# Performance work log

Measured on AMD Instinct MI355X. Metric: run time of the kernel, lower is better.

## Reference

```python
import jax, jax.numpy as jnp
import numpy as np

N, E, F, HID, HEADS, G = 20000, 320000, 64, 64, 4, 64
HC = HEADS * HID  # 256
NHID, NOUT = 256, 128
INV_SQRT2 = 0.7071067811865476


def _gat(x, src, dst, W, a_s, a_d, bias):
    # GATConv (v1), eval mode (no dropout); src/dst already include self-loops (PyG default)
    H, C = a_s.shape
    h = (x @ W).reshape(-1, H, C)  # [N,H,C]
    al_s = jnp.einsum('nhc,hc->nh', h, a_s)
    al_d = jnp.einsum('nhc,hc->nh', h, a_d)
    e = jax.nn.leaky_relu(al_s[src] + al_d[dst], 0.2)  # [Etot,H]
    m = jax.ops.segment_max(e, dst, num_segments=N)
    ex = jnp.exp(e - m[dst])
    den = jax.ops.segment_sum(ex, dst, num_segments=N)
    coef = ex / den[dst]  # softmax over incoming edges per target node
    out = jax.ops.segment_sum(h[src] * coef[:, :, None], dst, num_segments=N)
    return out.reshape(-1, H * C) + bias


def _bn(h, g, b):
    # BatchNorm1d, training-mode stats (biased var), eps=1e-5
    mu = h.mean(axis=0)
    var = h.var(axis=0)
    return g * (h - mu) * jax.lax.rsqrt(var + 1e-5) + b


def _block(x, src, dst, W1, a1s, a1d, b1, g1, be1, W2, a2s, a2d, b2, g2, be2, Wr, br, Wf, bf):
    h = jax.nn.relu(_bn(_gat(x, src, dst, W1, a1s, a1d, b1), g1, be1))
    h = jax.nn.relu(_bn(_gat(h, src, dst, W2, a2s, a2d, b2), g2, be2))
    res = x @ Wr + br
    return ((h + res) * INV_SQRT2) @ Wf + bf


def setup_inputs():
    ks = iter(jax.random.split(jax.random.key(0), 64))
    def rn(shape, scale=0.05):
        return jax.random.normal(next(ks), shape, dtype=jnp.float32) * scale
    inp = {}
    inp['x'] = jax.random.normal(next(ks), (N, F), dtype=jnp.float32)
    inp['edge_index'] = jax.random.randint(next(ks), (2, E), 0, N, dtype=jnp.int32)
    inp['batch'] = jnp.sort(jax.random.randint(next(ks), (N,), 0, G, dtype=jnp.int32))
    for b, cin in enumerate([F, HID]):
        p = 'b%d_' % b
        inp[p + 'W1'] = rn((cin, HC)); inp[p + 'a1s'] = rn((HEADS, HID)); inp[p + 'a1d'] = rn((HEADS, HID))
        inp[p + 'b1'] = jnp.zeros((HC,), jnp.float32)
        inp[p + 'g1'] = jnp.ones((HC,), jnp.float32); inp[p + 'be1'] = jnp.zeros((HC,), jnp.float32)
        inp[p + 'W2'] = rn((HC, HC)); inp[p + 'a2s'] = rn((1, HC)); inp[p + 'a2d'] = rn((1, HC))
        inp[p + 'b2'] = jnp.zeros((HC,), jnp.float32)
        inp[p + 'g2'] = jnp.ones((HC,), jnp.float32); inp[p + 'be2'] = jnp.zeros((HC,), jnp.float32)
        inp[p + 'Wr'] = rn((cin, HC)); inp[p + 'br'] = jnp.zeros((HC,), jnp.float32)
        inp[p + 'Wf'] = rn((HC, HID)); inp[p + 'bf'] = jnp.zeros((HID,), jnp.float32)
    inp['Wh1'] = rn((HID, NHID)); inp['bh1'] = jnp.zeros((NHID,), jnp.float32)
    inp['Wh2'] = rn((NHID, NOUT)); inp['bh2'] = jnp.zeros((NOUT,), jnp.float32)
    return inp


def reference(x, edge_index, batch,
              b0_W1, b0_a1s, b0_a1d, b0_b1, b0_g1, b0_be1, b0_W2, b0_a2s, b0_a2d, b0_b2, b0_g2, b0_be2, b0_Wr, b0_br, b0_Wf, b0_bf,
              b1_W1, b1_a1s, b1_a1d, b1_b1, b1_g1, b1_be1, b1_W2, b1_a2s, b1_a2d, b1_b2, b1_g2, b1_be2, b1_Wr, b1_br, b1_Wf, b1_bf,
              Wh1, bh1, Wh2, bh2):
    loops = jnp.arange(N, dtype=edge_index.dtype)
    src = jnp.concatenate([edge_index[0], loops])
    dst = jnp.concatenate([edge_index[1], loops])
    x = _block(x, src, dst, b0_W1, b0_a1s, b0_a1d, b0_b1, b0_g1, b0_be1, b0_W2, b0_a2s, b0_a2d, b0_b2, b0_g2, b0_be2, b0_Wr, b0_br, b0_Wf, b0_bf)
    x = _block(x, src, dst, b1_W1, b1_a1s, b1_a1d, b1_b1, b1_g1, b1_be1, b1_W2, b1_a2s, b1_a2d, b1_b2, b1_g2, b1_be2, b1_Wr, b1_br, b1_Wf, b1_bf)
    cnt = jax.ops.segment_sum(jnp.ones((N,), x.dtype), batch, num_segments=G)
    pooled = jax.ops.segment_sum(x, batch, num_segments=G) / jnp.maximum(cnt, 1.0)[:, None]
    h = jax.nn.relu(pooled @ Wh1 + bh1)
    return h @ Wh2 + bh2
```

## Files before the change

### kernel.cpp

```cpp
#include <hip/hip_runtime.h>

#define N_NODES 20000
#define N_EDGES 320000
#define ETOT (N_EDGES + N_NODES)
#define G_GROUPS 64
#define BN_BLOCKS 256
#define BN_BANKS 8

typedef __attribute__((ext_vector_type(8))) short bf16x8;
typedef __attribute__((ext_vector_type(4))) float f32x4;

__device__ __forceinline__ unsigned short f2bf(float f) {
    unsigned int u = __float_as_uint(f);
    u += 0x7fffu + ((u >> 16) & 1u);
    return (unsigned short)(u >> 16);
}
__device__ __forceinline__ float bf2f(unsigned short v) {
    return __uint_as_float(((unsigned int)v) << 16);
}
__device__ __forceinline__ unsigned int pack2bf(float a, float b) {
    return (unsigned int)f2bf(a) | ((unsigned int)f2bf(b) << 16);
}


__global__ __launch_bounds__(256) void k_hist(const int* __restrict__ ei, int* __restrict__ counts) {
    int e = blockIdx.x * 256 + threadIdx.x;
    if (e >= ETOT) return;
    int dst = (e < N_EDGES) ? ei[N_EDGES + e] : (e - N_EDGES);
    atomicAdd(&counts[dst], 1);
}

__global__ __launch_bounds__(1024) void k_scan(const int* __restrict__ counts, int* __restrict__ offs,
                                               int* __restrict__ cursor) {
    __shared__ int sdata[1024];
    const int t = threadIdx.x;
    const int chunk = (N_NODES + 1023) / 1024;
    int base = t * chunk;
    int s = 0;
    for (int i = 0; i < chunk; i++) { int idx = base + i; if (idx < N_NODES) s += counts[idx]; }
    sdata[t] = s;
    __syncthreads();
    for (int off = 1; off < 1024; off <<= 1) {
        int v = (t >= off) ? sdata[t - off] : 0;
        __syncthreads();
        sdata[t] += v;
        __syncthreads();
    }
    int prefix = (t == 0) ? 0 : sdata[t - 1];
    for (int i = 0; i < chunk; i++) {
        int idx = base + i;
        if (idx < N_NODES) {
            int cv = counts[idx];
            offs[idx] = prefix;
            cursor[idx] = prefix;
            prefix += cv;
        }
    }
    if (t == 1023) offs[N_NODES] = sdata[1023];
}

__global__ __launch_bounds__(256) void k_scatter(const int* __restrict__ ei, int* __restrict__ cursor,
                                                 int* __restrict__ csr_src) {
    int e = blockIdx.x * 256 + threadIdx.x;
    if (e >= ETOT) return;
    int src = (e < N_EDGES) ? ei[e] : (e - N_EDGES);
    int dst = (e < N_EDGES) ? ei[N_EDGES + e] : (e - N_EDGES);
    int p = atomicAdd(&cursor[dst], 1);
    csr_src[p] = src;
}


__global__ __launch_bounds__(256) void k_prepB_all(const float* __restrict__ W2a, const float* __restrict__ W2b,
                                                   const float* __restrict__ W1a, const float* __restrict__ Wra,
                                                   const float* __restrict__ W1b, const float* __restrict__ Wrb,
                                                   unsigned short* __restrict__ B2a, unsigned short* __restrict__ B2b,
                                                   unsigned short* __restrict__ B1a, unsigned short* __restrict__ Bra,
                                                   unsigned short* __restrict__ B1b, unsigned short* __restrict__ Brb) {
    int b = blockIdx.x;
    const float* W;
    unsigned short* Bf;
    int s0;
    if (b < 32) { W = W2a; Bf = B2a; s0 = b; }
    else if (b < 64) { W = W2b; Bf = B2b; s0 = b - 32; }
    else if (b < 72) { W = W1a; Bf = B1a; s0 = b - 64; }
    else if (b < 80) { W = Wra; Bf = Bra; s0 = b - 72; }
    else if (b < 88) { W = W1b; Bf = B1b; s0 = b - 80; }
    else { W = Wrb; Bf = Brb; s0 = b - 88; }
    int s = s0 * 256 + threadIdx.x;
    int l = s & 63;
    int nt = (s >> 6) & 15;
    int kt = s >> 10;
    int n = nt * 16 + (l & 15);
    int kb = kt * 32 + (l >> 4) * 8;
    float v[8];
    #pragma unroll
    for (int j = 0; j < 8; j++) v[j] = W[(kb + j) * 256 + n];
    uint4 q = {pack2bf(v[0], v[1]), pack2bf(v[2], v[3]), pack2bf(v[4], v[5]), pack2bf(v[6], v[7])};
    *(uint4*)(Bf + s * 8) = q;
}


__global__ __launch_bounds__(256) void k_gemm64_dual(const float* __restrict__ x,
                                                     const unsigned short* __restrict__ Bf1,
                                                     const unsigned short* __restrict__ Bfr,
                                                     const float* __restrict__ br,
                                                     const float* __restrict__ a_s, const float* __restrict__ a_d,
                                                     unsigned short* __restrict__ hbf, float* __restrict__ res,
                                                     float* __restrict__ alS, float* __restrict__ alD) {
    const int rb = blockIdx.x >> 2, cs = blockIdx.x & 3;
    const int row0 = rb * 64;
    const int nrows = min(64, N_NODES - row0);
    const int t = threadIdx.x;
    const int w = t >> 6;
    const int l = t & 63;
    const int quad = l >> 4;
    const int colLocal = l & 15;
    __shared__ unsigned short As[8 * 64 * 8];
    __shared__ float alsm[4][64], aldm[4][64];

    const int ntg = cs * 4 + w;
    bf16x8 b1f[2], brf[2];
    #pragma unroll
    for (int kt = 0; kt < 2; kt++) {
        b1f[kt] = *(const bf16x8*)(Bf1 + ((kt * 16 + ntg) * 64 + l) * 8);
        brf[kt] = *(const bf16x8*)(Bfr + ((kt * 16 + ntg) * 64 + l) * 8);
    }

    #pragma unroll
    for (int gi = 0; gi < 2; gi++) {
        int g = 2 * w + gi;
        int kt = g >> 2, mt = g & 3;
        int sm = mt * 16 + (l & 15);
        int koff = kt * 32 + (l >> 4) * 8;
        float4 v0 = {0.f, 0.f, 0.f, 0.f}, v1 = {0.f, 0.f, 0.f, 0.f};
        if (sm < nrows) {
            v0 = *(const float4*)(x + (row0 + sm) * 64 + koff);
            v1 = *(const float4*)(x + (row0 + sm) * 64 + koff + 4);
        }
        uint4 q = {pack2bf(v0.x, v0.y), pack2bf(v0.z, v0.w), pack2bf(v1.x, v1.y), pack2bf(v1.z, v1.w)};
        *(uint4*)(As + (g * 64 + l) * 8) = q;
    }
    __syncthreads();

    f32x4 acc1[4], acc2[4];
    #pragma unroll
    for (int mt = 0; mt < 4; mt++) {
        acc1[mt] = (f32x4){0.f, 0.f, 0.f, 0.f};
        acc2[mt] = (f32x4){0.f, 0.f, 0.f, 0.f};
    }
    #pragma unroll
    for (int kt = 0; kt < 2; kt++) {
        #pragma unroll
        for (int mt = 0; mt < 4; mt++) {
            bf16x8 af = *(const bf16x8*)(As + ((kt * 4 + mt) * 64 + l) * 8);
            acc1[mt] = __builtin_amdgcn_mfma_f32_16x16x32_bf16(af, b1f[kt], acc1[mt], 0, 0, 0);
            acc2[mt] = __builtin_amdgcn_mfma_f32_16x16x32_bf16(af, brf[kt], acc2[mt], 0, 0, 0);
        }
    }

    const int col = cs * 64 + w * 16 + colLocal;
    const float brv = br[col];
    const float asv = a_s[col];
    const float adv = a_d[col];
    #pragma unroll
    for (int mt = 0; mt < 4; mt++) {
        #pragma unroll
        for (int r = 0; r < 4; r++) {
            float v1 = acc1[mt][r];
            int lr = mt * 16 + quad * 4 + r;
            bool ok = lr < nrows;
            int row = row0 + lr;
            if (ok) {
                hbf[row * 256 + col] = f2bf(v1);
                res[row * 256 + col] = acc2[mt][r] + brv;
            }
            float ps = v1 * asv, pd = v1 * adv;
            #pragma unroll
            for (int off = 1; off < 16; off <<= 1) {
                ps += __shfl_xor(ps, off);
                pd += __shfl_xor(pd, off);
            }
            if (colLocal == 0) {
                alsm[w][lr] = ps;
                aldm[w][lr] = pd;
            }
        }
    }
    __syncthreads();
    if (t < 64 && t < nrows) {
        float s = (alsm[0][t] + alsm[1][t]) + (alsm[2][t] + alsm[3][t]);
        float d = (aldm[0][t] + aldm[1][t]) + (aldm[2][t] + aldm[3][t]);
        alS[(row0 + t) * 4 + cs] = s;
        alD[(row0 + t) * 4 + cs] = d;
    }
}


template <int H>
__global__ __launch_bounds__(256) void k_agg(const unsigned short* __restrict__ hbf, const float* __restrict__ alS,
                                             const float* __restrict__ alD, const int* __restrict__ offs,
                                             const int* __restrict__ csr_src, const float* __restrict__ bias,
                                             float* __restrict__ out) {
    const int node = __builtin_amdgcn_readfirstlane(blockIdx.x * 4 + (threadIdx.x >> 6));
    const int lane = threadIdx.x & 63;
    const int head = (H == 4) ? (lane >> 4) : 0;
    float ald;
    if (H == 4) {
        float4 d4 = *(const float4*)(alD + node * 4);
        ald = (head == 0) ? d4.x : (head == 1) ? d4.y : (head == 2) ? d4.z : d4.w;
    } else {
        ald = alD[node];
    }
    const int e0 = offs[node], e1 = offs[node + 1];
    const unsigned short* hp = hbf + lane * 4;
    float den = 0.f, a0 = 0.f, a1 = 0.f, a2 = 0.f, a3 = 0.f;
    int e = e0;
    for (; e + 16 <= e1; e += 16) {
        int s[16];
        #pragma unroll
        for (int i = 0; i < 16; i++) s[i] = csr_src[e + i];
        ushort4 hq[16];
        #pragma unroll
        for (int i = 0; i < 16; i++) hq[i] = *(const ushort4*)(hp + s[i] * 256);
        float w[16];
        #pragma unroll
        for (int i = 0; i < 16; i++) {
            float v;
            if (H == 4) {
                float4 s4 = *(const float4*)(alS + s[i] * 4);
                float as = (head == 0) ? s4.x : (head == 1) ? s4.y : (head == 2) ? s4.z : s4.w;
                v = as + ald;
            } else {
                v = alS[s[i]] + ald;
            }
            v = (v > 0.f) ? v : 0.2f * v;
            w[i] = __expf(v);
        }
        #pragma unroll
        for (int i = 0; i < 16; i++) {
            den += w[i];
            a0 += w[i] * bf2f(hq[i].x); a1 += w[i] * bf2f(hq[i].y);
            a2 += w[i] * bf2f(hq[i].z); a3 += w[i] * bf2f(hq[i].w);
        }
    }
    for (; e < e1; e++) {
        int s = csr_src[e];
        float v;
        if (H == 4) {
            float4 s4 = *(const float4*)(alS + s * 4);
            float as = (head == 0) ? s4.x : (head == 1) ? s4.y : (head == 2) ? s4.z : s4.w;
            v = as + ald;
        } else {
            v = alS[s] + ald;
        }
        v = (v > 0.f) ? v : 0.2f * v;
        float w = __expf(v);
        ushort4 hq = *(const ushort4*)(hp + s * 256);
        den += w;
        a0 += w * bf2f(hq.x); a1 += w * bf2f(hq.y); a2 += w * bf2f(hq.z); a3 += w * bf2f(hq.w);
    }
    float inv = 1.f / den;
    const float4 bv = *(const float4*)(bias + lane * 4);
    float4 o = {a0 * inv + bv.x, a1 * inv + bv.y, a2 * inv + bv.z, a3 * inv + bv.w};
    *(float4*)(out + node * 256 + lane * 4) = o;
}


__global__ __launch_bounds__(256) void k_bnstats_fin(const float* __restrict__ x, float* __restrict__ sumR,
                                                     float* __restrict__ sumsqR, const float* __restrict__ g,
                                                     const float* __restrict__ be, float* __restrict__ scale,
                                                     float* __restrict__ shift, int* __restrict__ counter,
                                                     float* __restrict__ zS, float* __restrict__ zD) {
    const int c = threadIdx.x;
    const int bank = blockIdx.x & (BN_BANKS - 1);
    if (zS) {
        int idx = blockIdx.x * 256 + c;
        if (idx < N_NODES) { zS[idx] = 0.f; zD[idx] = 0.f; }
    }
    float s = 0.f, q = 0.f;
    int r = blockIdx.x;
    for (; r + 3 * BN_BLOCKS < N_NODES; r += 4 * BN_BLOCKS) {
        float v0 = x[r * 256 + c];
        float v1 = x[(r + BN_BLOCKS) * 256 + c];
        float v2 = x[(r + 2 * BN_BLOCKS) * 256 + c];
        float v3 = x[(r + 3 * BN_BLOCKS) * 256 + c];
        s += (v0 + v1) + (v2 + v3);
        q += (v0 * v0 + v1 * v1) + (v2 * v2 + v3 * v3);
    }
    for (; r < N_NODES; r += BN_BLOCKS) {
        float v = x[r * 256 + c];
        s += v; q += v * v;
    }
    atomicAdd(&sumR[bank * 256 + c], s);
    atomicAdd(&sumsqR[bank * 256 + c], q);
    __threadfence();
    __syncthreads();
    __shared__ int lastFlag;
    if (c == 0) lastFlag = (atomicAdd(counter, 1) == (int)gridDim.x - 1);
    __syncthreads();
    if (lastFlag) {
        float S = 0.f, Q = 0.f;
        #pragma unroll
        for (int k = 0; k < BN_BANKS; k++) {
            S += atomicAdd(&sumR[k * 256 + c], 0.f);
            Q += atomicAdd(&sumsqR[k * 256 + c], 0.f);
        }
        float mu = S * (1.f / N_NODES);
        float var = Q * (1.f / N_NODES) - mu * mu;
        float sc = g[c] * rsqrtf(var + 1e-5f);
        scale[c] = sc;
        shift[c] = be[c] - mu * sc;
        #pragma unroll
        for (int k = 0; k < BN_BANKS; k++) {
            sumR[k * 256 + c] = 0.f;
            sumsqR[k * 256 + c] = 0.f;
        }
        if (c == 0) *counter = 0;
    }
}


__global__ __launch_bounds__(256) void k_gemm256_mfma(const float* __restrict__ A, const float* __restrict__ scale,
                                                      const float* __restrict__ shift,
                                                      const unsigned short* __restrict__ Bf,
                                                      const float* __restrict__ a_s, const float* __restrict__ a_d,
                                                      unsigned short* __restrict__ C, float* __restrict__ alS2,
                                                      float* __restrict__ alD2) {
    const int rb = blockIdx.x >> 2, cs = blockIdx.x & 3;
    const int row0 = rb * 64;
    const int nrows = min(64, N_NODES - row0);
    const int t = threadIdx.x;
    const int w = t >> 6;
    const int l = t & 63;
    const int quad = l >> 4;
    const int colLocal = l & 15;
    __shared__ unsigned short As[2 * 4 * 64 * 8];
    __shared__ float scs[256], shs[256];
    scs[t] = scale[t];
    shs[t] = shift[t];

    const int ntg = cs * 4 + w;
    bf16x8 bfrag[8];
    #pragma unroll
    for (int kt = 0; kt < 8; kt++)
        bfrag[kt] = *(const bf16x8*)(Bf + ((kt * 16 + ntg) * 64 + l) * 8);

    f32x4 acc[4];
    #pragma unroll
    for (int mt = 0; mt < 4; mt++) acc[mt] = (f32x4){0.f, 0.f, 0.f, 0.f};

    const int smt = (t >> 6) & 3;
    const int sm = smt * 16 + (l & 15);
    const int skoff = (l >> 4) * 8;

    for (int kc = 0; kc < 4; kc++) {
        __syncthreads();
        #pragma unroll
        for (int kt2 = 0; kt2 < 2; kt2++) {
            int k = kc * 64 + kt2 * 32 + skoff;
            float4 v0 = {0.f, 0.f, 0.f, 0.f}, v1 = {0.f, 0.f, 0.f, 0.f};
            if (sm < nrows) {
                v0 = *(const float4*)(A + (row0 + sm) * 256 + k);
                v1 = *(const float4*)(A + (row0 + sm) * 256 + k + 4);
                v0.x = fmaxf(v0.x * scs[k + 0] + shs[k + 0], 0.f);
                v0.y = fmaxf(v0.y * scs[k + 1] + shs[k + 1], 0.f);
                v0.z = fmaxf(v0.z * scs[k + 2] + shs[k + 2], 0.f);
                v0.w = fmaxf(v0.w * scs[k + 3] + shs[k + 3], 0.f);
                v1.x = fmaxf(v1.x * scs[k + 4] + shs[k + 4], 0.f);
                v1.y = fmaxf(v1.y * scs[k + 5] + shs[k + 5], 0.f);
                v1.z = fmaxf(v1.z * scs[k + 6] + shs[k + 6], 0.f);
                v1.w = fmaxf(v1.w * scs[k + 7] + shs[k + 7], 0.f);
            }
            uint4 q = {pack2bf(v0.x, v0.y), pack2bf(v0.z, v0.w), pack2bf(v1.x, v1.y), pack2bf(v1.z, v1.w)};
            *(uint4*)(As + ((kt2 * 4 + smt) * 64 + l) * 8) = q;
        }
        __syncthreads();
        #pragma unroll
        for (int kt2 = 0; kt2 < 2; kt2++) {
            int ktg = kc * 2 + kt2;
            #pragma unroll
            for (int mt = 0; mt < 4; mt++) {
                bf16x8 af = *(const bf16x8*)(As + ((kt2 * 4 + mt) * 64 + l) * 8);
                acc[mt] = __builtin_amdgcn_mfma_f32_16x16x32_bf16(af, bfrag[ktg], acc[mt], 0, 0, 0);
            }
        }
    }

    const int col = cs * 64 + w * 16 + colLocal;
    const float asv = a_s[col];
    const float adv = a_d[col];
    #pragma unroll
    for (int mt = 0; mt < 4; mt++) {
        #pragma unroll
        for (int r = 0; r < 4; r++) {
            float v = acc[mt][r];
            int lr = mt * 16 + quad * 4 + r;
            bool ok = lr < nrows;
            int row = row0 + lr;
            if (ok) C[row * 256 + col] = f2bf(v);
            float ps = v * asv, pd = v * adv;
            #pragma unroll
            for (int off = 1; off < 16; off <<= 1) {
                ps += __shfl_xor(ps, off);
                pd += __shfl_xor(pd, off);
            }
            if (colLocal == 0 && ok) {
                atomicAdd(&alS2[row], ps);
                atomicAdd(&alD2[row], pd);
            }
        }
    }
}


__global__ __launch_bounds__(256) void k_gemm_final(const float* __restrict__ A, const float* __restrict__ scale,
                                                    const float* __restrict__ shift, const float* __restrict__ res,
                                                    const float* __restrict__ B, const float* __restrict__ bias,
                                                    float* __restrict__ y) {
    const int row0 = blockIdx.x * 32;
    const int t = threadIdx.x;
    const float INVS = 0.70710678118654752440f;
    __shared__ float xs[32 * 36];
    __shared__ float bs[32 * 64];
    __shared__ float scs[256], shs[256];
    scs[t] = scale[t];
    shs[t] = shift[t];
    const int rf = (t & 15) | ((t >> 7) << 4);
    const int cf = (t >> 4) & 7;
    const int c0 = (t & 15) * 4;
    const int r0 = (t >> 4) * 2;
    float acc[2][4] = {};
    for (int k0 = 0; k0 < 256; k0 += 32) {
        __syncthreads();
        {
            int kcol = k0 + cf * 4;
            int gi = (row0 + rf) * 256 + kcol;
            float4 v = *(const float4*)(A + gi);
            float4 rv = *(const float4*)(res + gi);
            xs[(cf * 4 + 0) * 36 + rf] = (fmaxf(v.x * scs[kcol + 0] + shs[kcol + 0], 0.f) + rv.x) * INVS;
            xs[(cf * 4 + 1) * 36 + rf] = (fmaxf(v.y * scs[kcol + 1] + shs[kcol + 1], 0.f) + rv.y) * INVS;
            xs[(cf * 4 + 2) * 36 + rf] = (fmaxf(v.z * scs[kcol + 2] + shs[kcol + 2], 0.f) + rv.z) * INVS;
            xs[(cf * 4 + 3) * 36 + rf] = (fmaxf(v.w * scs[kcol + 3] + shs[kcol + 3], 0.f) + rv.w) * INVS;
        }
        {
            int cc = (t & 15) * 4;
            int k = t >> 4;
            #pragma unroll
            for (int pass = 0; pass < 2; pass++, k += 16) {
                *(float4*)(bs + k * 64 + cc) = *(const float4*)(B + (k0 + k) * 64 + cc);
            }
        }
        __syncthreads();
        #pragma unroll 8
        for (int k = 0; k < 32; k++) {
            float2 av = *(const float2*)(xs + k * 36 + r0);
            float4 bv = *(const float4*)(bs + k * 64 + c0);
            acc[0][0] += av.x * bv.x; acc[0][1] += av.x * bv.y;
            acc[0][2] += av.x * bv.z; acc[0][3] += av.x * bv.w;
            acc[1][0] += av.y * bv.x; acc[1][1] += av.y * bv.y;
            acc[1][2] += av.y * bv.z; acc[1][3] += av.y * bv.w;
        }
    }
    float4 bv = *(const float4*)(bias + c0);
    #pragma unroll
    for (int i = 0; i < 2; i++) {
        int gr = row0 + r0 + i;
        float4 o = {acc[i][0] + bv.x, acc[i][1] + bv.y, acc[i][2] + bv.z, acc[i][3] + bv.w};
        *(float4*)(y + gr * 64 + c0) = o;
    }
}


__global__ __launch_bounds__(256) void k_pool_head(const float* __restrict__ x, const int* __restrict__ batch,
                                                   const float* __restrict__ Wh1, const float* __restrict__ bh1,
                                                   const float* __restrict__ Wh2, const float* __restrict__ bh2,
                                                   float* __restrict__ out) {
    const int g = blockIdx.x;
    const int t = threadIdx.x;
    int lo = 0, hi = N_NODES;
    while (lo < hi) { int mid = (lo + hi) >> 1; if (batch[mid] < g) lo = mid + 1; else hi = mid; }
    int start = lo;
    hi = N_NODES;
    while (lo < hi) { int mid = (lo + hi) >> 1; if (batch[mid] < g + 1) lo = mid + 1; else hi = mid; }
    int end = lo;
    float cnt = (float)(end - start);

    __shared__ float part[256];
    __shared__ float p[64];
    __shared__ float hrow[256];
    const int c = t & 63;
    float s = 0.f;
    for (int r = start + (t >> 6); r < end; r += 4) s += x[r * 64 + c];
    part[t] = s;
    __syncthreads();
    if (t < 64) {
        float v = part[t] + part[t + 64] + part[t + 128] + part[t + 192];
        p[t] = v / fmaxf(cnt, 1.f);
    }
    __syncthreads();
    float a = bh1[t];
    #pragma unroll 8
    for (int k = 0; k < 64; k++) a += p[k] * Wh1[k * 256 + t];
    hrow[t] = fmaxf(a, 0.f);
    __syncthreads();
    if (t < 128) {
        float o = bh2[t];
        #pragma unroll 8
        for (int k = 0; k < 256; k++) o += hrow[k] * Wh2[k * 128 + t];
        out[g * 128 + t] = o;
    }
}


extern "C" void kernel_launch(void* const* d_in, const int* in_sizes, int n_in,
                              void* d_out, int out_size, void* d_ws, size_t ws_size,
                              hipStream_t stream) {
    (void)in_sizes; (void)n_in; (void)out_size; (void)ws_size;
    const float* x0 = (const float*)d_in[0];
    const int* ei = (const int*)d_in[1];
    const int* batch = (const int*)d_in[2];
    const float* Wh1 = (const float*)d_in[35];
    const float* bh1 = (const float*)d_in[36];
    const float* Wh2 = (const float*)d_in[37];
    const float* bh2 = (const float*)d_in[38];

    char* p = (char*)d_ws;
    auto alloc = [&](size_t bytes) -> void* {
        void* r = (void*)p;
        p += (bytes + 255) & ~(size_t)255;
        return r;
    };
    int* counts = (int*)alloc((size_t)N_NODES * 4);
    float* sumR = (float*)alloc(BN_BANKS * 256 * 4);
    float* sumsqR = (float*)alloc(BN_BANKS * 256 * 4);
    int* bncnt = (int*)alloc(256);
    const size_t zero_bytes = (((size_t)N_NODES * 4 + 255) & ~(size_t)255) + BN_BANKS * 256 * 4 * 2 + 256;
    int* offs = (int*)alloc((size_t)(N_NODES + 1) * 4);
    int* cursor = (int*)alloc((size_t)N_NODES * 4);
    int* csr_src = (int*)alloc((size_t)ETOT * 4);
    float* alS = (float*)alloc((size_t)N_NODES * 4 * 4);
    float* alD = (float*)alloc((size_t)N_NODES * 4 * 4);
    float* alS2 = (float*)alloc((size_t)N_NODES * 4);
    float* alD2 = (float*)alloc((size_t)N_NODES * 4);
    float* scaleb = (float*)alloc(1024);
    float* shiftb = (float*)alloc(1024);
    unsigned short* hbuf = (unsigned short*)alloc((size_t)N_NODES * 256 * 2);
    float* obuf = (float*)alloc((size_t)N_NODES * 256 * 4);
    float* rbuf = (float*)alloc((size_t)N_NODES * 256 * 4);
    float* xout = (float*)alloc((size_t)N_NODES * 64 * 4);
    unsigned short* Bf2_0 = (unsigned short*)alloc(256 * 256 * 2);
    unsigned short* Bf2_1 = (unsigned short*)alloc(256 * 256 * 2);
    unsigned short* Bf1_0 = (unsigned short*)alloc(64 * 256 * 2);
    unsigned short* Bfr_0 = (unsigned short*)alloc(64 * 256 * 2);
    unsigned short* Bf1_1 = (unsigned short*)alloc(64 * 256 * 2);
    unsigned short* Bfr_1 = (unsigned short*)alloc(64 * 256 * 2);

    hipMemsetAsync(counts, 0, zero_bytes, stream);
    k_hist<<<(ETOT + 255) / 256, 256, 0, stream>>>(ei, counts);
    k_scan<<<1, 1024, 0, stream>>>(counts, offs, cursor);
    k_scatter<<<(ETOT + 255) / 256, 256, 0, stream>>>(ei, cursor, csr_src);
    k_prepB_all<<<96, 256, 0, stream>>>((const float*)d_in[3 + 6], (const float*)d_in[19 + 6],
                                        (const float*)d_in[3 + 0], (const float*)d_in[3 + 12],
                                        (const float*)d_in[19 + 0], (const float*)d_in[19 + 12],
                                        Bf2_0, Bf2_1, Bf1_0, Bfr_0, Bf1_1, Bfr_1);

    const int tile64_blocks = ((N_NODES + 63) / 64) * 4;
    const int node_blocks = N_NODES / 4;
    const int final_blocks = N_NODES / 32;

    auto run_block = [&](const float* xin, int base, const unsigned short* Bf2,
                         const unsigned short* Bf1, const unsigned short* Bfr) {
        const float* a1s = (const float*)d_in[base + 1];
        const float* a1d = (const float*)d_in[base + 2];
        const float* b1 = (const float*)d_in[base + 3];
        const float* g1 = (const float*)d_in[base + 4];
        const float* be1 = (const float*)d_in[base + 5];
        const float* a2s = (const float*)d_in[base + 7];
        const float* a2d = (const float*)d_in[base + 8];
        const float* b2 = (const float*)d_in[base + 9];
        const float* g2 = (const float*)d_in[base + 10];
        const float* be2 = (const float*)d_in[base + 11];
        const float* br = (const float*)d_in[base + 13];
        const float* Wf = (const float*)d_in[base + 14];
        const float* bf = (const float*)d_in[base + 15];

        k_gemm64_dual<<<tile64_blocks, 256, 0, stream>>>(xin, Bf1, Bfr, br, a1s, a1d, hbuf, rbuf, alS, alD);
        k_agg<4><<<node_blocks, 256, 0, stream>>>(hbuf, alS, alD, offs, csr_src, b1, obuf);
        k_bnstats_fin<<<BN_BLOCKS, 256, 0, stream>>>(obuf, sumR, sumsqR, g1, be1, scaleb, shiftb, bncnt, alS2, alD2);
        k_gemm256_mfma<<<tile64_blocks, 256, 0, stream>>>(obuf, scaleb, shiftb, Bf2, a2s, a2d, hbuf, alS2, alD2);
        k_agg<1><<<node_blocks, 256, 0, stream>>>(hbuf, alS2, alD2, offs, csr_src, b2, obuf);
        k_bnstats_fin<<<BN_BLOCKS, 256, 0, stream>>>(obuf, sumR, sumsqR, g2, be2, scaleb, shiftb, bncnt, nullptr, nullptr);
        k_gemm_final<<<final_blocks, 256, 0, stream>>>(obuf, scaleb, shiftb, rbuf, Wf, bf, xout);
    };

    run_block(x0, 3, Bf2_0, Bf1_0, Bfr_0);
    run_block(xout, 19, Bf2_1, Bf1_1, Bfr_1);

    k_pool_head<<<G_GROUPS, 256, 0, stream>>>(xout, batch, Wh1, bh1, Wh2, bh2, (float*)d_out);
}
```

Measured before the change: 591.0 us.

## Fuse BatchNorm statistics into GAT aggregation kernel with two-level completion counter

Removes the separate BN-stats kernel. Each aggregation block now reduces its four nodes' outputs and squares in shared memory and atomically adds them into banked partial sums. A per-bank counter followed by a master counter picks the last block, which finalizes scale and shift. This avoids re-reading the 20000x256 fp32 aggregation output and saves one launch per layer. In exchange, all 5000 blocks now issue 512 float atomics each, which may cause contention on the 8 banks.

```diff
diff --git a/kernel.cpp b/kernel.cpp
--- a/kernel.cpp
+++ b/kernel.cpp
@@ -4,7 +4,6 @@
 #define N_EDGES 320000
 #define ETOT (N_EDGES + N_NODES)
 #define G_GROUPS 64
-#define BN_BLOCKS 256
 #define BN_BANKS 8
 
 typedef __attribute__((ext_vector_type(8))) short bf16x8;
@@ -197,13 +196,24 @@
 
 
 template <int H>
-__global__ __launch_bounds__(256) void k_agg(const unsigned short* __restrict__ hbf, const float* __restrict__ alS,
-                                             const float* __restrict__ alD, const int* __restrict__ offs,
-                                             const int* __restrict__ csr_src, const float* __restrict__ bias,
-                                             float* __restrict__ out) {
+__global__ __launch_bounds__(256) void k_agg_bn(const unsigned short* __restrict__ hbf,
+                                               const float* __restrict__ alS, const float* __restrict__ alD,
+                                               const int* __restrict__ offs, const int* __restrict__ csr_src,
+                                               const float* __restrict__ bias, float* __restrict__ out,
+                                               float* __restrict__ sumR, float* __restrict__ sumsqR,
+                                               const float* __restrict__ g, const float* __restrict__ be,
+                                               float* __restrict__ scale, float* __restrict__ shift,
+                                               int* __restrict__ cntBank, int* __restrict__ cntMaster,
+                                               float* __restrict__ zS, float* __restrict__ zD) {
     const int node = __builtin_amdgcn_readfirstlane(blockIdx.x * 4 + (threadIdx.x >> 6));
-    const int lane = threadIdx.x & 63;
+    const int t = threadIdx.x;
+    const int lane = t & 63;
+    const int w = t >> 6;
     const int head = (H == 4) ? (lane >> 4) : 0;
+    __shared__ float lsum[4][256], lqsum[4][256];
+
+    if (H == 4 && lane == 0) { zS[node] = 0.f; zD[node] = 0.f; }
+
     float ald;
     if (H == 4) {
         float4 d4 = *(const float4*)(alD + node * 4);
@@ -222,7 +232,7 @@
         ushort4 hq[16];
         #pragma unroll
         for (int i = 0; i < 16; i++) hq[i] = *(const ushort4*)(hp + s[i] * 256);
-        float w[16];
+        float wq[16];
         #pragma unroll
         for (int i = 0; i < 16; i++) {
             float v;
@@ -234,13 +244,13 @@
                 v = alS[s[i]] + ald;
             }
             v = (v > 0.f) ? v : 0.2f * v;
-            w[i] = __expf(v);
+            wq[i] = __expf(v);
         }
         #pragma unroll
         for (int i = 0; i < 16; i++) {
-            den += w[i];
-            a0 += w[i] * bf2f(hq[i].x); a1 += w[i] * bf2f(hq[i].y);
-            a2 += w[i] * bf2f(hq[i].z); a3 += w[i] * bf2f(hq[i].w);
+            den += wq[i];
+            a0 += wq[i] * bf2f(hq[i].x); a1 += wq[i] * bf2f(hq[i].y);
+            a2 += wq[i] * bf2f(hq[i].z); a3 += wq[i] * bf2f(hq[i].w);
         }
     }
     for (; e < e1; e++) {
@@ -254,51 +264,40 @@
             v = alS[s] + ald;
         }
         v = (v > 0.f) ? v : 0.2f * v;
-        float w = __expf(v);
+        float wv = __expf(v);
         ushort4 hq = *(const ushort4*)(hp + s * 256);
-        den += w;
-        a0 += w * bf2f(hq.x); a1 += w * bf2f(hq.y); a2 += w * bf2f(hq.z); a3 += w * bf2f(hq.w);
+        den += wv;
+        a0 += wv * bf2f(hq.x); a1 += wv * bf2f(hq.y); a2 += wv * bf2f(hq.z); a3 += wv * bf2f(hq.w);
     }
     float inv = 1.f / den;
     const float4 bv = *(const float4*)(bias + lane * 4);
     float4 o = {a0 * inv + bv.x, a1 * inv + bv.y, a2 * inv + bv.z, a3 * inv + bv.w};
     *(float4*)(out + node * 256 + lane * 4) = o;
-}
-
-
-__global__ __launch_bounds__(256) void k_bnstats_fin(const float* __restrict__ x, float* __restrict__ sumR,
-                                                     float* __restrict__ sumsqR, const float* __restrict__ g,
-                                                     const float* __restrict__ be, float* __restrict__ scale,
-                                                     float* __restrict__ shift, int* __restrict__ counter,
-                                                     float* __restrict__ zS, float* __restrict__ zD) {
-    const int c = threadIdx.x;
+
+    *(float4*)(&lsum[w][lane * 4]) = o;
+    float4 q2 = {o.x * o.x, o.y * o.y, o.z * o.z, o.w * o.w};
+    *(float4*)(&lqsum[w][lane * 4]) = q2;
+    __syncthreads();
     const int bank = blockIdx.x & (BN_BANKS - 1);
-    if (zS) {
-        int idx = blockIdx.x * 256 + c;
-        if (idx < N_NODES) { zS[idx] = 0.f; zD[idx] = 0.f; }
-    }
-    float s = 0.f, q = 0.f;
-    int r = blockIdx.x;
-    for (; r + 3 * BN_BLOCKS < N_NODES; r += 4 * BN_BLOCKS) {
-        float v0 = x[r * 256 + c];
-        float v1 = x[(r + BN_BLOCKS) * 256 + c];
-        float v2 = x[(r + 2 * BN_BLOCKS) * 256 + c];
-        float v3 = x[(r + 3 * BN_BLOCKS) * 256 + c];
-        s += (v0 + v1) + (v2 + v3);
-        q += (v0 * v0 + v1 * v1) + (v2 * v2 + v3 * v3);
-    }
-    for (; r < N_NODES; r += BN_BLOCKS) {
-        float v = x[r * 256 + c];
-        s += v; q += v * v;
-    }
-    atomicAdd(&sumR[bank * 256 + c], s);
-    atomicAdd(&sumsqR[bank * 256 + c], q);
+    {
+        float s4 = (lsum[0][t] + lsum[1][t]) + (lsum[2][t] + lsum[3][t]);
+        float q4 = (lqsum[0][t] + lqsum[1][t]) + (lqsum[2][t] + lqsum[3][t]);
+        atomicAdd(&sumR[bank * 256 + t], s4);
+        atomicAdd(&sumsqR[bank * 256 + t], q4);
+    }
     __threadfence();
     __syncthreads();
     __shared__ int lastFlag;
-    if (c == 0) lastFlag = (atomicAdd(counter, 1) == (int)gridDim.x - 1);
+    if (t == 0) {
+        int done = atomicAdd(&cntBank[bank * 16], 1);
+        int lastInBank = (done == (int)(gridDim.x / BN_BANKS) - 1);
+        int m = 0;
+        if (lastInBank) m = atomicAdd(cntMaster, 1);
+        lastFlag = (lastInBank && m == BN_BANKS - 1);
+    }
     __syncthreads();
     if (lastFlag) {
+        const int c = t;
         float S = 0.f, Q = 0.f;
         #pragma unroll
         for (int k = 0; k < BN_BANKS; k++) {
@@ -315,7 +314,8 @@
             sumR[k * 256 + c] = 0.f;
             sumsqR[k * 256 + c] = 0.f;
         }
-        if (c == 0) *counter = 0;
+        if (c < BN_BANKS) cntBank[c * 16] = 0;
+        if (c == 0) *cntMaster = 0;
     }
 }
 
@@ -533,8 +533,10 @@
     int* counts = (int*)alloc((size_t)N_NODES * 4);
     float* sumR = (float*)alloc(BN_BANKS * 256 * 4);
     float* sumsqR = (float*)alloc(BN_BANKS * 256 * 4);
-    int* bncnt = (int*)alloc(256);
-    const size_t zero_bytes = (((size_t)N_NODES * 4 + 255) & ~(size_t)255) + BN_BANKS * 256 * 4 * 2 + 256;
+    int* cntBank = (int*)alloc(BN_BANKS * 16 * 4);
+    int* cntMaster = (int*)alloc(256);
+    const size_t zero_bytes = (((size_t)N_NODES * 4 + 255) & ~(size_t)255) + BN_BANKS * 256 * 4 * 2 +
+                              BN_BANKS * 16 * 4 + 256;
     int* offs = (int*)alloc((size_t)(N_NODES + 1) * 4);
     int* cursor = (int*)alloc((size_t)N_NODES * 4);
     int* csr_src = (int*)alloc((size_t)ETOT * 4);
@@ -585,11 +587,13 @@
         const float* bf = (const float*)d_in[base + 15];
 
         k_gemm64_dual<<<tile64_blocks, 256, 0, stream>>>(xin, Bf1, Bfr, br, a1s, a1d, hbuf, rbuf, alS, alD);
-        k_agg<4><<<node_blocks, 256, 0, stream>>>(hbuf, alS, alD, offs, csr_src, b1, obuf);
-        k_bnstats_fin<<<BN_BLOCKS, 256, 0, stream>>>(obuf, sumR, sumsqR, g1, be1, scaleb, shiftb, bncnt, alS2, alD2);
+        k_agg_bn<4><<<node_blocks, 256, 0, stream>>>(hbuf, alS, alD, offs, csr_src, b1, obuf,
+                                                     sumR, sumsqR, g1, be1, scaleb, shiftb,
+                                                     cntBank, cntMaster, alS2, alD2);
         k_gemm256_mfma<<<tile64_blocks, 256, 0, stream>>>(obuf, scaleb, shiftb, Bf2, a2s, a2d, hbuf, alS2, alD2);
-        k_agg<1><<<node_blocks, 256, 0, stream>>>(hbuf, alS2, alD2, offs, csr_src, b2, obuf);
-        k_bnstats_fin<<<BN_BLOCKS, 256, 0, stream>>>(obuf, sumR, sumsqR, g2, be2, scaleb, shiftb, bncnt, nullptr, nullptr);
+        k_agg_bn<1><<<node_blocks, 256, 0, stream>>>(hbuf, alS2, alD2, offs, csr_src, b2, obuf,
+                                                     sumR, sumsqR, g2, be2, scaleb, shiftb,
+                                                     cntBank, cntMaster, nullptr, nullptr);
         k_gemm_final<<<final_blocks, 256, 0, stream>>>(obuf, scaleb, shiftb, rbuf, Wf, bf, xout);
     };
 
```

Result: slower. 2.263 ms (+283.0%).
